# Kernel tuning notes

Measured on AMD Instinct MI355X. Metric: run time of the kernel, lower is better.

The kernel has to match this reference:

```python
import jax, jax.numpy as jnp
import numpy as np

N_MAP, N_ACT, B, E_PER, D = 131072, 1024, 16, 16384, 128
MAP_PER, ACT_PER = N_MAP // B, N_ACT // B
E = B * E_PER
EPS = 1e-5  # torch GroupNorm default eps


def _gn(x, g, b):
    # GroupNorm(1, C) on [N, C]: per-row normalization over channels
    m = jnp.mean(x, -1, keepdims=True)
    v = jnp.mean((x - m) ** 2, -1, keepdims=True)
    return (x - m) * jax.lax.rsqrt(v + EPS) * g + b


def _lin_gn(x, W, g, b, act=True):
    # LaneGCN Linear: nn.Linear(bias=False) -> GroupNorm(1, n_out) -> optional ReLU
    y = _gn(x @ W.T, g, b)
    return jax.nn.relu(y) if act else y


def setup_inputs() -> dict:
    key = jax.random.key(0)
    keys = iter(jax.random.split(key, 64))
    nrm = lambda shape, s=1.0: jax.random.normal(next(keys), shape, jnp.float32) * s
    uni = lambda shape, s=1.0: jax.random.uniform(next(keys), shape, jnp.float32) * s
    inp = {}
    inp['feat'] = nrm((N_MAP, D))
    inp['turn'] = nrm((N_MAP, 2))
    inp['control'] = uni((N_MAP,))
    inp['intersect'] = uni((N_MAP,))
    inp['map_ctrs'] = uni((N_MAP, 2), 100.0)
    inp['actors'] = nrm((N_ACT, D))
    inp['actor_ctrs'] = uni((N_ACT, 2), 100.0)
    # fixed within-scene edge list (stands in for the distance-threshold nonzero)
    rng = np.random.default_rng(0)
    hi = np.concatenate([rng.integers(b * MAP_PER, (b + 1) * MAP_PER, E_PER) for b in range(B)])
    wi = np.concatenate([rng.integers(b * ACT_PER, (b + 1) * ACT_PER, E_PER) for b in range(B)])
    inp['hi'] = jnp.asarray(hi, jnp.int32)
    inp['wi'] = jnp.asarray(wi, jnp.int32)
    # parameters
    W = lambda *s: nrm(s, 0.02)
    g_ = lambda *s: 1.0 + nrm(s, 0.05)
    b_ = lambda *s: nrm(s, 0.05)
    inp['meta_W'], inp['meta_g'], inp['meta_b'] = W(D, D + 4), g_(D), b_(D)
    inp['dW1'], inp['db1'] = W(2, D, 2), b_(2, D)
    inp['dW2'], inp['dg2'], inp['dbt2'] = W(2, D, D), g_(2, D), b_(2, D)
    inp['qW'], inp['qg'], inp['qb'] = W(2, D, D), g_(2, D), b_(2, D)
    inp['cW1'], inp['cg1'], inp['cb1'] = W(2, D, 3 * D), g_(2, D), b_(2, D)
    inp['cW2'] = W(2, D, D)
    inp['aW'] = W(2, D, D)
    inp['ng_g'], inp['ng_b'] = g_(2, D), b_(2, D)
    inp['lW'], inp['lg'], inp['lb'] = W(2, D, D), g_(2, D), b_(2, D)
    return inp


def reference(feat, turn, control, intersect, map_ctrs, actors, actor_ctrs, hi, wi,
              meta_W, meta_g, meta_b, dW1, db1, dW2, dg2, dbt2, qW, qg, qb,
              cW1, cg1, cb1, cW2, aW, ng_g, ng_b, lW, lg, lb):
    # meta fuse: concat(feat, turn, control, intersect) -> Linear+GN+ReLU
    meta = jnp.concatenate([feat, turn, control[:, None], intersect[:, None]], axis=1)
    feat = _lin_gn(meta, meta_W, meta_g, meta_b)
    for i in range(2):  # two Att blocks
        res = feat
        # dist branch: raw ctr offsets -> Linear(2,n_ctx)+ReLU -> Linear+GN+ReLU
        d = map_ctrs[hi] - actor_ctrs[wi]                       # [E, 2]
        d = jax.nn.relu(d @ dW1[i].T + db1[i])                  # [E, D]
        d = _lin_gn(d, dW2[i], dg2[i], dbt2[i])
        q = _lin_gn(feat[hi], qW[i], qg[i], qb[i])              # query on gathered agts
        c = jnp.concatenate([d, q, actors[wi]], axis=1)         # [E, 3D]
        c = _lin_gn(c, cW1[i], cg1[i], cb1[i])
        c = c @ cW2[i].T                                        # bias-free Linear
        a = feat @ aW[i].T                                      # self path, bias-free
        a = a.at[hi].add(c)                                     # scatter-add messages
        a = jax.nn.relu(_gn(a, ng_g[i], ng_b[i]))
        a = _lin_gn(a, lW[i], lg[i], lb[i], act=False)
        feat = jax.nn.relu(a + res)                             # use_relu=True
    return feat
```

## Files before the change

kernel.cpp:

```cpp
#include <hip/hip_runtime.h>
#include <stdint.h>

typedef unsigned short u16;
typedef __bf16 bf16x8 __attribute__((ext_vector_type(8)));
typedef float f32x4 __attribute__((ext_vector_type(4)));

#define MFMA(a, b, c) __builtin_amdgcn_mfma_f32_16x16x32_bf16(a, b, c, 0, 0, 0)

__device__ __forceinline__ u16 f2bf(float f) {
    union { float f; unsigned u; } v; v.f = f;
    unsigned r = v.u + 0x7fffu + ((v.u >> 16) & 1u);
    return (u16)(r >> 16);
}
__device__ __forceinline__ float bf2f(u16 h) {
    union { unsigned u; float f; } v; v.u = ((unsigned)h) << 16; return v.f;
}
__device__ __forceinline__ bf16x8 as_frag(uint4 u) {
    union { uint4 u; bf16x8 b; } v; v.u = u; return v.b;
}
__device__ __forceinline__ bf16x8 ldg_frag(const u16* p) {
    return as_frag(*reinterpret_cast<const uint4*>(p));
}
__device__ __forceinline__ int rowmap(int t, int i) {
    return 32 * (t >> 1) + 8 * (i >> 2) + 4 * (t & 1) + (i & 3);
}

template <int SRC_LDU>
__device__ __forceinline__ void stage128(const u16* __restrict__ src, u16* dst, int tid, int nt) {
    for (int c = tid; c < 2048; c += nt) {
        int row = c >> 4, j = c & 15;
        int js = (j & 8) | ((j ^ row) & 7);
        *reinterpret_cast<uint4*>(dst + row * 128 + js * 8) =
            *reinterpret_cast<const uint4*>(src + row * SRC_LDU + j * 8);
    }
}
__device__ __forceinline__ bf16x8 lds_w(const u16* base, int row, int byteoff) {
    int off = row * 256 + (byteoff ^ ((row & 7) << 4));
    return as_frag(*reinterpret_cast<const uint4*>(reinterpret_cast<const char*>(base) + off));
}

template <int KT>
__device__ __forceinline__ void gemm_acc(const bf16x8* a, const u16* __restrict__ W, int ldw,
                                         f32x4* acc, int c16, int q4) {
#pragma unroll
    for (int n = 0; n < 8; n++) {
        const u16* wp = W + (size_t)(n * 16 + c16) * ldw + q4 * 8;
#pragma unroll
        for (int k = 0; k < KT; k++) {
            bf16x8 b = ldg_frag(wp + k * 32);
            acc[n] = MFMA(a[k], b, acc[n]);
        }
    }
}

__device__ __forceinline__ void gn_t(f32x4* acc, const float* __restrict__ gb, bool relu, int q4) {
    float s = 0.f, s2 = 0.f;
#pragma unroll
    for (int t = 0; t < 8; t++)
#pragma unroll
        for (int r = 0; r < 4; r++) { float x = acc[t][r]; s += x; s2 = fmaf(x, x, s2); }
    s += __shfl_xor(s, 16, 64); s += __shfl_xor(s, 32, 64);
    s2 += __shfl_xor(s2, 16, 64); s2 += __shfl_xor(s2, 32, 64);
    float mean = s * (1.f / 128.f);
    float var = fmaf(s2, 1.f / 128.f, -mean * mean);
    float rstd = rsqrtf(var + 1e-5f);
#pragma unroll
    for (int t = 0; t < 8; t++) {
        const float4* g4 = reinterpret_cast<const float4*>(gb + (t * 16 + q4 * 4) * 2);
        float4 p01 = g4[0], p23 = g4[1];
        float gv[4] = {p01.x, p01.z, p23.x, p23.z};
        float bv[4] = {p01.y, p01.w, p23.y, p23.w};
#pragma unroll
        for (int r = 0; r < 4; r++) {
            float y = fmaf((acc[t][r] - mean) * rstd, gv[r], bv[r]);
            acc[t][r] = relu ? fmaxf(y, 0.f) : y;
        }
    }
}

__device__ __forceinline__ bf16x8 pack_frag(f32x4 lo, f32x4 hi) {
    union { u16 s[8]; bf16x8 b; } t;
#pragma unroll
    for (int j = 0; j < 4; j++) { t.s[j] = f2bf(lo[j]); t.s[4 + j] = f2bf(hi[j]); }
    return t.b;
}

__device__ __forceinline__ void gn_c(f32x4* acc, const float* __restrict__ g,
                                     const float* __restrict__ b, bool relu, int c16) {
    float gs[8], bs[8];
#pragma unroll
    for (int n = 0; n < 8; n++) { gs[n] = g[n * 16 + c16]; bs[n] = b[n * 16 + c16]; }
#pragma unroll
    for (int r = 0; r < 4; r++) {
        float s = 0.f, s2 = 0.f;
#pragma unroll
        for (int n = 0; n < 8; n++) { float x = acc[n][r]; s += x; s2 = fmaf(x, x, s2); }
#pragma unroll
        for (int m = 1; m < 16; m <<= 1) { s += __shfl_xor(s, m, 64); s2 += __shfl_xor(s2, m, 64); }
        float mean = s * (1.f / 128.f);
        float var = fmaf(s2, 1.f / 128.f, -mean * mean);
        float rstd = rsqrtf(var + 1e-5f);
#pragma unroll
        for (int n = 0; n < 8; n++) {
            float y = fmaf((acc[n][r] - mean) * rstd, gs[n], bs[n]);
            acc[n][r] = relu ? fmaxf(y, 0.f) : y;
        }
    }
}

__global__ __launch_bounds__(256) void k_prep(
    const float* __restrict__ dW2s, const float* __restrict__ qWs, const float* __restrict__ cW1s,
    const float* __restrict__ cW2s, const float* __restrict__ aWs, const float* __restrict__ lWs,
    const float* __restrict__ metaW,
    const float* __restrict__ dW1s, const float* __restrict__ db1s,
    const float* __restrict__ dg2s, const float* __restrict__ dbt2s,
    const float* __restrict__ qgs, const float* __restrict__ qbs,
    const float* __restrict__ cg1s, const float* __restrict__ cb1s,
    u16* __restrict__ o_dW2p, u16* __restrict__ o_qWp, u16* __restrict__ o_cW10,
    u16* __restrict__ o_cW1q, u16* __restrict__ o_cW1a,
    u16* __restrict__ o_cW2, u16* __restrict__ o_aW, u16* __restrict__ o_lW,
    u16* __restrict__ o_mWf, float* __restrict__ o_mWe,
    float* __restrict__ o_dw1p, float* __restrict__ o_gb) {
    int idx = blockIdx.x * 256 + threadIdx.x;
    if (idx >= 281600) return;
    if (idx < 32768) {
        int i = idx >> 14, rem = idx & 16383, ro = rem >> 7, col = rem & 127;
        o_dW2p[idx] = f2bf(dW2s[i * 16384 + rowmap(ro >> 4, ro & 15) * 128 + col]);
    } else if (idx < 65536) {
        int j = idx - 32768, i = j >> 14, rem = j & 16383, ro = rem >> 7, col = rem & 127;
        o_qWp[j] = f2bf(qWs[i * 16384 + rowmap(ro >> 4, ro & 15) * 128 + col]);
    } else if (idx < 98304) {
        int j = idx - 65536, i = j >> 14, rem = j & 16383, ro = rem >> 7, col = rem & 127;
        o_cW10[j] = f2bf(cW1s[i * 49152 + rowmap(ro >> 4, ro & 15) * 384 + col]);
    } else if (idx < 131072) {
        int j = idx - 98304, i = j >> 14, rem = j & 16383, ro = rem >> 7, col = rem & 127;
        o_cW1q[j] = f2bf(cW1s[i * 49152 + rowmap(ro >> 4, ro & 15) * 384 + 128 + col]);
    } else if (idx < 163840) {
        int j = idx - 131072, i = j >> 14, rem = j & 16383, ro = rem >> 7, col = rem & 127;
        o_cW1a[j] = f2bf(cW1s[i * 49152 + rowmap(ro >> 4, ro & 15) * 384 + 256 + col]);
    } else if (idx < 196608) { int j = idx - 163840; o_cW2[j] = f2bf(cW2s[j]); }
    else if (idx < 229376) { int j = idx - 196608; o_aW[j] = f2bf(aWs[j]); }
    else if (idx < 262144) { int j = idx - 229376; o_lW[j] = f2bf(lWs[j]); }
    else if (idx < 278528) { int j = idx - 262144; o_mWf[j] = f2bf(metaW[(j >> 7) * 132 + (j & 127)]); }
    else if (idx < 279040) { int j = idx - 278528; o_mWe[j] = metaW[(j >> 2) * 132 + 128 + (j & 3)]; }
    else if (idx < 280064) {
        int j = idx - 279040, i = j >> 9, col = (j >> 2) & 127, t = j & 3;
        float v = (t == 0) ? dW1s[i * 256 + col * 2]
                : (t == 1) ? dW1s[i * 256 + col * 2 + 1]
                : (t == 2) ? db1s[i * 128 + col] : 0.f;
        o_dw1p[j] = v;
    } else {
        int j = idx - 280064;
        int tb = j >> 9, rem = j & 511, i = rem >> 8, q = rem & 255, o = q >> 1, f = q & 1;
        const float* gsrc = (tb == 0) ? dg2s : (tb == 1) ? qgs : cg1s;
        const float* bsrc = (tb == 0) ? dbt2s : (tb == 1) ? qbs : cb1s;
        int src = i * 128 + rowmap(o >> 4, o & 15);
        o_gb[j] = f ? bsrc[src] : gsrc[src];
    }
}

__global__ __launch_bounds__(256) void k_meta(
    const float* __restrict__ feat, const float* __restrict__ turn,
    const float* __restrict__ ctrl, const float* __restrict__ inter,
    const u16* __restrict__ mWf, const float* __restrict__ mWe,
    const float* __restrict__ g, const float* __restrict__ b, u16* __restrict__ out) {
    int lane = threadIdx.x & 63, wv = threadIdx.x >> 6;
    int c16 = lane & 15, q4 = lane >> 4;
    int m0 = (blockIdx.x * 4 + wv) * 16;
    bf16x8 a[4];
    const float* xr = feat + (size_t)(m0 + c16) * 128 + q4 * 8;
#pragma unroll
    for (int k = 0; k < 4; k++) {
        float4 u0 = *reinterpret_cast<const float4*>(xr + k * 32);
        float4 u1 = *reinterpret_cast<const float4*>(xr + k * 32 + 4);
        union { u16 s[8]; bf16x8 b; } t;
        t.s[0] = f2bf(u0.x); t.s[1] = f2bf(u0.y); t.s[2] = f2bf(u0.z); t.s[3] = f2bf(u0.w);
        t.s[4] = f2bf(u1.x); t.s[5] = f2bf(u1.y); t.s[6] = f2bf(u1.z); t.s[7] = f2bf(u1.w);
        a[k] = t.b;
    }
    f32x4 acc[8] = {};
    gemm_acc<4>(a, mWf, 128, acc, c16, q4);
#pragma unroll
    for (int r = 0; r < 4; r++) {
        int row = m0 + q4 * 4 + r;
        float t0 = turn[2 * row], t1 = turn[2 * row + 1];
        float cv = ctrl[row], iv = inter[row];
#pragma unroll
        for (int n = 0; n < 8; n++) {
            int col = n * 16 + c16;
            float4 we = reinterpret_cast<const float4*>(mWe)[col];
            acc[n][r] += t0 * we.x + t1 * we.y + cv * we.z + iv * we.w;
        }
    }
    gn_c(acc, g, b, true, c16);
#pragma unroll
    for (int r = 0; r < 4; r++) {
        size_t row = m0 + q4 * 4 + r;
#pragma unroll
        for (int n = 0; n < 8; n++) out[row * 128 + n * 16 + c16] = f2bf(acc[n][r]);
    }
}

__global__ __launch_bounds__(256) void k_act(
    const float* __restrict__ actors, const u16* __restrict__ cW1ap, u16* __restrict__ ac_out) {
    int lane = threadIdx.x & 63, wv = threadIdx.x >> 6;
    int c16 = lane & 15, q4 = lane >> 4;
    int b = (int)blockIdx.x;
    int i = b >> 4;
    int row = ((b & 15) * 4 + wv) * 16 + c16;
    const float* xr = actors + (size_t)row * 128 + q4 * 8;
    bf16x8 f[4];
#pragma unroll
    for (int k = 0; k < 4; k++) {
        union { u16 s[8]; uint4 u; } t;
#pragma unroll
        for (int j = 0; j < 8; j++) t.s[j] = f2bf(xr[k * 32 + j]);
        f[k] = as_frag(t.u);
    }
    const u16* Wp = cW1ap + i * 16384;
    f32x4 acc[8] = {};
#pragma unroll
    for (int k = 0; k < 4; k++)
#pragma unroll
        for (int t = 0; t < 8; t++) {
            bf16x8 a = ldg_frag(Wp + (size_t)(t * 16 + c16) * 128 + k * 32 + q4 * 8);
            acc[t] = MFMA(a, f[k], acc[t]);
        }
    u16* dst = ac_out + (size_t)i * 131072 + (size_t)row * 128 + q4 * 8;
#pragma unroll
    for (int T = 0; T < 4; T++) {
        bf16x8 p = pack_frag(acc[2 * T], acc[2 * T + 1]);
        union { bf16x8 b; uint4 u; } v; v.b = p;
        *reinterpret_cast<uint4*>(dst + T * 32) = v.u;
    }
}

__global__ __launch_bounds__(256) void k_nodeA(
    const u16* __restrict__ featb, const u16* __restrict__ qWp, const u16* __restrict__ aW,
    const float* __restrict__ gb_q, const u16* __restrict__ cW1qp,
    u16* __restrict__ qc_out, float* __restrict__ a_out) {
    int lane = threadIdx.x & 63, wv = threadIdx.x >> 6;
    int c16 = lane & 15, q4 = lane >> 4;
    int m0 = (blockIdx.x * 4 + wv) * 16;
    bf16x8 f[4];
    const u16* xr = featb + (size_t)(m0 + c16) * 128 + q4 * 8;
#pragma unroll
    for (int k = 0; k < 4; k++) f[k] = ldg_frag(xr + k * 32);
    f32x4 acca[8] = {};
    gemm_acc<4>(f, aW, 128, acca, c16, q4);
#pragma unroll
    for (int r = 0; r < 4; r++) {
        size_t row = m0 + q4 * 4 + r;
#pragma unroll
        for (int n = 0; n < 8; n++) a_out[row * 128 + n * 16 + c16] = acca[n][r];
    }
    f32x4 accq[8] = {};
#pragma unroll
    for (int k = 0; k < 4; k++)
#pragma unroll
        for (int t = 0; t < 8; t++) {
            bf16x8 a = ldg_frag(qWp + (size_t)(t * 16 + c16) * 128 + k * 32 + q4 * 8);
            accq[t] = MFMA(a, f[k], accq[t]);
        }
    gn_t(accq, gb_q, true, q4);
    bf16x8 qf[4];
#pragma unroll
    for (int k = 0; k < 4; k++) qf[k] = pack_frag(accq[2 * k], accq[2 * k + 1]);
    f32x4 acc2[8] = {};
#pragma unroll
    for (int k = 0; k < 4; k++)
#pragma unroll
        for (int t = 0; t < 8; t++) {
            bf16x8 a = ldg_frag(cW1qp + (size_t)(t * 16 + c16) * 128 + k * 32 + q4 * 8);
            acc2[t] = MFMA(a, qf[k], acc2[t]);
        }
    u16* dst = qc_out + (size_t)(m0 + c16) * 128 + q4 * 8;
#pragma unroll
    for (int T = 0; T < 4; T++) {
        bf16x8 p = pack_frag(acc2[2 * T], acc2[2 * T + 1]);
        union { bf16x8 b; uint4 u; } v; v.b = p;
        *reinterpret_cast<uint4*>(dst + T * 32) = v.u;
    }
}

__global__ __launch_bounds__(256) void k_edge(
    const int* __restrict__ hi, const int* __restrict__ wi,
    const float* __restrict__ mctr, const float* __restrict__ actr,
    const float* __restrict__ dw1p, const u16* __restrict__ dW2p,
    const float* __restrict__ gb_d2,
    const u16* __restrict__ qc, const u16* __restrict__ ac,
    const u16* __restrict__ cW10p, const float* __restrict__ gb_c1,
    const u16* __restrict__ cW2, float* __restrict__ a_out) {
    __shared__ u16 s0[16384];
    int tid = threadIdx.x;
    int lane = tid & 63, wv = tid >> 6;
    int c16 = lane & 15, q4 = lane >> 4;
    int bid = (int)blockIdx.x;
    bid = (bid & 7) * 256 + (bid >> 3);
    int ebase = bid * 128 + wv * 32;
    int h0 = hi[ebase + c16], w0 = wi[ebase + c16];
    int h1 = hi[ebase + 16 + c16], w1 = wi[ebase + 16 + c16];
    stage128<128>(dW2p, s0, tid, 256);
    union F8 { bf16x8 b; uint4 u; u16 s[8]; };
    F8 qg0[4], qg1[4], ag0[4], ag1[4];
#pragma unroll
    for (int T = 0; T < 4; T++) {
        qg0[T].b = ldg_frag(qc + (size_t)h0 * 128 + T * 32 + q4 * 8);
        qg1[T].b = ldg_frag(qc + (size_t)h1 * 128 + T * 32 + q4 * 8);
        ag0[T].b = ldg_frag(ac + (size_t)w0 * 128 + T * 32 + q4 * 8);
        ag1[T].b = ldg_frag(ac + (size_t)w1 * 128 + T * 32 + q4 * 8);
    }
    float dx0 = mctr[2 * h0] - actr[2 * w0], dy0 = mctr[2 * h0 + 1] - actr[2 * w0 + 1];
    float dx1 = mctr[2 * h1] - actr[2 * w1], dy1 = mctr[2 * h1 + 1] - actr[2 * w1 + 1];
    bf16x8 bd0[4], bd1[4];
    const float4* w4p = reinterpret_cast<const float4*>(dw1p);
#pragma unroll
    for (int k = 0; k < 4; k++) {
        union { u16 s[8]; uint4 u; } t0, t1;
#pragma unroll
        for (int j = 0; j < 8; j++) {
            float4 w4 = w4p[k * 32 + q4 * 8 + j];
            t0.s[j] = f2bf(fmaxf(fmaf(dx0, w4.x, fmaf(dy0, w4.y, w4.z)), 0.f));
            t1.s[j] = f2bf(fmaxf(fmaf(dx1, w4.x, fmaf(dy1, w4.y, w4.z)), 0.f));
        }
        bd0[k] = as_frag(t0.u); bd1[k] = as_frag(t1.u);
    }
    __syncthreads();
    f32x4 accA[8] = {}, accB[8] = {};
#pragma unroll
    for (int k = 0; k < 4; k++)
#pragma unroll
        for (int t = 0; t < 8; t++) {
            bf16x8 a = lds_w(s0, t * 16 + c16, k * 64 + q4 * 16);
            accA[t] = MFMA(a, bd0[k], accA[t]);
            accB[t] = MFMA(a, bd1[k], accB[t]);
        }
    gn_t(accA, gb_d2, true, q4);
    gn_t(accB, gb_d2, true, q4);
    bf16x8 d2f0[4], d2f1[4];
#pragma unroll
    for (int k = 0; k < 4; k++) {
        d2f0[k] = pack_frag(accA[2 * k], accA[2 * k + 1]);
        d2f1[k] = pack_frag(accB[2 * k], accB[2 * k + 1]);
    }
    __syncthreads();
    stage128<128>(cW10p, s0, tid, 256);
    __syncthreads();
    f32x4 cA[8] = {}, cB[8] = {};
#pragma unroll
    for (int k = 0; k < 4; k++)
#pragma unroll
        for (int t = 0; t < 8; t++) {
            bf16x8 a = lds_w(s0, t * 16 + c16, k * 64 + q4 * 16);
            cA[t] = MFMA(a, d2f0[k], cA[t]);
            cB[t] = MFMA(a, d2f1[k], cB[t]);
        }
#pragma unroll
    for (int t = 0; t < 8; t++) {
        int T = t >> 1, base = 4 * (t & 1);
#pragma unroll
        for (int r = 0; r < 4; r++) {
            cA[t][r] += bf2f(qg0[T].s[base + r]) + bf2f(ag0[T].s[base + r]);
            cB[t][r] += bf2f(qg1[T].s[base + r]) + bf2f(ag1[T].s[base + r]);
        }
    }
    gn_t(cA, gb_c1, true, q4);
    gn_t(cB, gb_c1, true, q4);
    bf16x8 ba0[4], ba1[4];
#pragma unroll
    for (int k = 0; k < 4; k++) {
        ba0[k] = pack_frag(cA[2 * k], cA[2 * k + 1]);
        ba1[k] = pack_frag(cB[2 * k], cB[2 * k + 1]);
    }
    __syncthreads();
    stage128<128>(cW2, s0, tid, 256);
    __syncthreads();
    f32x4 oA[8] = {}, oB[8] = {};
#pragma unroll
    for (int k = 0; k < 4; k++)
#pragma unroll
        for (int n = 0; n < 8; n++) {
            bf16x8 b = lds_w(s0, n * 16 + c16, k * 64 + q4 * 16);
            oA[n] = MFMA(ba0[k], b, oA[n]);
            oB[n] = MFMA(ba1[k], b, oB[n]);
        }
#pragma unroll
    for (int r = 0; r < 4; r++) {
        int hr0 = hi[ebase + q4 * 4 + r];
        int hr1 = hi[ebase + 16 + q4 * 4 + r];
        float* dst0 = a_out + (size_t)hr0 * 128 + c16;
        float* dst1 = a_out + (size_t)hr1 * 128 + c16;
#pragma unroll
        for (int n = 0; n < 8; n++) {
            unsafeAtomicAdd(dst0 + n * 16, oA[n][r]);
            unsafeAtomicAdd(dst1 + n * 16, oB[n][r]);
        }
    }
}

__global__ __launch_bounds__(256) void k_nodeB(
    const float* __restrict__ a_in, const float* __restrict__ gg, const float* __restrict__ gb,
    const u16* __restrict__ lW, const float* __restrict__ lg, const float* __restrict__ lb,
    const u16* __restrict__ res, u16* __restrict__ out_bf, float* __restrict__ out_f32) {
    int lane = threadIdx.x & 63, wv = threadIdx.x >> 6;
    int c16 = lane & 15, q4 = lane >> 4;
    int m0 = (blockIdx.x * 4 + wv) * 16;
    const float* xr = a_in + (size_t)(m0 + c16) * 128 + q4 * 8;
    float x[32];
#pragma unroll
    for (int k = 0; k < 4; k++) {
        float4 u0 = *reinterpret_cast<const float4*>(xr + k * 32);
        float4 u1 = *reinterpret_cast<const float4*>(xr + k * 32 + 4);
        x[k * 8 + 0] = u0.x; x[k * 8 + 1] = u0.y; x[k * 8 + 2] = u0.z; x[k * 8 + 3] = u0.w;
        x[k * 8 + 4] = u1.x; x[k * 8 + 5] = u1.y; x[k * 8 + 6] = u1.z; x[k * 8 + 7] = u1.w;
    }
    float s = 0.f, s2 = 0.f;
#pragma unroll
    for (int t = 0; t < 32; t++) { s += x[t]; s2 = fmaf(x[t], x[t], s2); }
    s += __shfl_xor(s, 16, 64); s += __shfl_xor(s, 32, 64);
    s2 += __shfl_xor(s2, 16, 64); s2 += __shfl_xor(s2, 32, 64);
    float mean = s * (1.f / 128.f);
    float var = fmaf(s2, 1.f / 128.f, -mean * mean);
    float rstd = rsqrtf(var + 1e-5f);
    bf16x8 a[4];
#pragma unroll
    for (int k = 0; k < 4; k++) {
        float4 g0 = *reinterpret_cast<const float4*>(gg + k * 32 + q4 * 8);
        float4 g1 = *reinterpret_cast<const float4*>(gg + k * 32 + q4 * 8 + 4);
        float4 b0 = *reinterpret_cast<const float4*>(gb + k * 32 + q4 * 8);
        float4 b1 = *reinterpret_cast<const float4*>(gb + k * 32 + q4 * 8 + 4);
        float gv[8] = {g0.x, g0.y, g0.z, g0.w, g1.x, g1.y, g1.z, g1.w};
        float bv[8] = {b0.x, b0.y, b0.z, b0.w, b1.x, b1.y, b1.z, b1.w};
        union { u16 s[8]; bf16x8 b; } t;
#pragma unroll
        for (int j = 0; j < 8; j++) {
            float y = fmaf((x[k * 8 + j] - mean) * rstd, gv[j], bv[j]);
            t.s[j] = f2bf(fmaxf(y, 0.f));
        }
        a[k] = t.b;
    }
    f32x4 acc[8] = {};
    gemm_acc<4>(a, lW, 128, acc, c16, q4);
    gn_c(acc, lg, lb, false, c16);
#pragma unroll
    for (int r = 0; r < 4; r++) {
        size_t row = m0 + q4 * 4 + r;
#pragma unroll
        for (int n = 0; n < 8; n++) {
            int col = n * 16 + c16;
            float y = acc[n][r] + bf2f(res[row * 128 + col]);
            y = fmaxf(y, 0.f);
            if (out_bf) out_bf[row * 128 + col] = f2bf(y);
            else out_f32[row * 128 + col] = y;
        }
    }
}

extern "C" void kernel_launch(void* const* d_in, const int* in_sizes, int n_in,
                              void* d_out, int out_size, void* d_ws, size_t ws_size,
                              hipStream_t stream) {
    const float* feat = (const float*)d_in[0];
    const float* turn = (const float*)d_in[1];
    const float* ctrl = (const float*)d_in[2];
    const float* inter = (const float*)d_in[3];
    const float* mctr = (const float*)d_in[4];
    const float* actors = (const float*)d_in[5];
    const float* actr = (const float*)d_in[6];
    const int* hi = (const int*)d_in[7];
    const int* wi = (const int*)d_in[8];
    const float* metaW = (const float*)d_in[9];
    const float* metag = (const float*)d_in[10];
    const float* metab = (const float*)d_in[11];
    const float* dW1 = (const float*)d_in[12];
    const float* db1 = (const float*)d_in[13];
    const float* dW2 = (const float*)d_in[14];
    const float* dg2 = (const float*)d_in[15];
    const float* dbt2 = (const float*)d_in[16];
    const float* qW = (const float*)d_in[17];
    const float* qg = (const float*)d_in[18];
    const float* qb = (const float*)d_in[19];
    const float* cW1 = (const float*)d_in[20];
    const float* cg1 = (const float*)d_in[21];
    const float* cb1 = (const float*)d_in[22];
    const float* cW2 = (const float*)d_in[23];
    const float* aW = (const float*)d_in[24];
    const float* ngg = (const float*)d_in[25];
    const float* ngb = (const float*)d_in[26];
    const float* lW = (const float*)d_in[27];
    const float* lg = (const float*)d_in[28];
    const float* lb = (const float*)d_in[29];

    char* ws = (char*)d_ws;
    u16* feat0 = (u16*)(ws);
    u16* feat1 = (u16*)(ws + 33554432);
    u16* qcbuf = (u16*)(ws + 67108864);
    u16* acbuf = (u16*)(ws + 100663296);
    u16* wdW2p = (u16*)(ws + 101187584);
    u16* wqWp = (u16*)(ws + 101253120);
    u16* wcW10 = (u16*)(ws + 101318656);
    u16* wcW1q = (u16*)(ws + 101384192);
    u16* wcW1a = (u16*)(ws + 101449728);
    u16* wcW2 = (u16*)(ws + 101515264);
    u16* waW = (u16*)(ws + 101580800);
    u16* wlW = (u16*)(ws + 101646336);
    u16* wmWf = (u16*)(ws + 101711872);
    float* wmWe = (float*)(ws + 101744640);
    float* wdw1p = (float*)(ws + 101746688);
    float* gball = (float*)(ws + 101750784);
    float* abuf = (float*)d_out;

    k_prep<<<1100, 256, 0, stream>>>(dW2, qW, cW1, cW2, aW, lW, metaW, dW1, db1,
                                     dg2, dbt2, qg, qb, cg1, cb1,
                                     wdW2p, wqWp, wcW10, wcW1q, wcW1a, wcW2, waW, wlW,
                                     wmWf, wmWe, wdw1p, gball);
    k_meta<<<2048, 256, 0, stream>>>(feat, turn, ctrl, inter, wmWf, wmWe, metag, metab, feat0);
    k_act<<<32, 256, 0, stream>>>(actors, wcW1a, acbuf);
    for (int i = 0; i < 2; i++) {
        const u16* fcur = i ? feat1 : feat0;
        k_nodeA<<<2048, 256, 0, stream>>>(fcur, wqWp + i * 16384, waW + i * 16384,
                                          gball + 512 + i * 256, wcW1q + i * 16384,
                                          qcbuf, abuf);
        k_edge<<<2048, 256, 0, stream>>>(hi, wi, mctr, actr, wdw1p + i * 512, wdW2p + i * 16384,
                                         gball + i * 256, qcbuf, acbuf + i * 131072,
                                         wcW10 + i * 16384, gball + 1024 + i * 256,
                                         wcW2 + i * 16384, abuf);
        k_nodeB<<<2048, 256, 0, stream>>>(abuf, ngg + i * 128, ngb + i * 128, wlW + i * 16384,
                                          lg + i * 128, lb + i * 128, fcur,
                                          i ? nullptr : feat1, i ? (float*)d_out : nullptr);
    }
}
```

Baseline: 704.1 us.

## Accumulate scatter buffer in bf16 with packed bf16 atomics, reuse feat buffers

The node accumulator `a` changes from fp32 to bf16. The self-path kernel writes bf16, and the edge kernel scatters messages with global_atomic_pk_add_bf16. Lane pairs exchange values by shuffle so each atomic carries two adjacent channels. This halves the number of atomic operations and the bytes moved through the scatter buffer and the following GroupNorm read. The buffer is aliased onto the idle feature ping-pong buffer, so the normalization kernel now updates it in place. The cost is accuracy: repeated bf16 rounding during accumulation can drift from the fp32 reference.

```diff
diff --git a/kernel.cpp b/kernel.cpp
--- a/kernel.cpp
+++ b/kernel.cpp
@@ -238,7 +238,7 @@
 __global__ __launch_bounds__(256) void k_nodeA(
     const u16* __restrict__ featb, const u16* __restrict__ qWp, const u16* __restrict__ aW,
     const float* __restrict__ gb_q, const u16* __restrict__ cW1qp,
-    u16* __restrict__ qc_out, float* __restrict__ a_out) {
+    u16* __restrict__ qc_out, u16* __restrict__ a_out) {
     int lane = threadIdx.x & 63, wv = threadIdx.x >> 6;
     int c16 = lane & 15, q4 = lane >> 4;
     int m0 = (blockIdx.x * 4 + wv) * 16;
@@ -252,7 +252,7 @@
     for (int r = 0; r < 4; r++) {
         size_t row = m0 + q4 * 4 + r;
 #pragma unroll
-        for (int n = 0; n < 8; n++) a_out[row * 128 + n * 16 + c16] = acca[n][r];
+        for (int n = 0; n < 8; n++) a_out[row * 128 + n * 16 + c16] = f2bf(acca[n][r]);
     }
     f32x4 accq[8] = {};
 #pragma unroll
@@ -290,7 +290,7 @@
     const float* __restrict__ gb_d2,
     const u16* __restrict__ qc, const u16* __restrict__ ac,
     const u16* __restrict__ cW10p, const float* __restrict__ gb_c1,
-    const u16* __restrict__ cW2, float* __restrict__ a_out) {
+    const u16* __restrict__ cW2, u16* __restrict__ a_out) {
     __shared__ u16 s0[16384];
     int tid = threadIdx.x;
     int lane = tid & 63, wv = tid >> 6;
@@ -388,31 +388,42 @@
     for (int r = 0; r < 4; r++) {
         int hr0 = hi[ebase + q4 * 4 + r];
         int hr1 = hi[ebase + 16 + q4 * 4 + r];
-        float* dst0 = a_out + (size_t)hr0 * 128 + c16;
-        float* dst1 = a_out + (size_t)hr1 * 128 + c16;
+        u16* d0 = a_out + (size_t)hr0 * 128 + (c16 & ~1);
+        u16* d1 = a_out + (size_t)hr1 * 128 + (c16 & ~1);
 #pragma unroll
         for (int n = 0; n < 8; n++) {
-            unsafeAtomicAdd(dst0 + n * 16, oA[n][r]);
-            unsafeAtomicAdd(dst1 + n * 16, oB[n][r]);
+            float pA = __shfl_xor(oA[n][r], 1, 64);
+            float pB = __shfl_xor(oB[n][r], 1, 64);
+            bool even = !(c16 & 1);
+            float loA = even ? oA[n][r] : pA, hiA = even ? pA : oA[n][r];
+            float loB = even ? oB[n][r] : pB, hiB = even ? pB : oB[n][r];
+            unsigned pkA = (unsigned)f2bf(loA) | ((unsigned)f2bf(hiA) << 16);
+            unsigned pkB = (unsigned)f2bf(loB) | ((unsigned)f2bf(hiB) << 16);
+            if ((n & 1) == (c16 & 1)) {
+                asm volatile("global_atomic_pk_add_bf16 %0, %1, off"
+                             :: "v"(d0 + n * 16), "v"(pkA) : "memory");
+                asm volatile("global_atomic_pk_add_bf16 %0, %1, off"
+                             :: "v"(d1 + n * 16), "v"(pkB) : "memory");
+            }
         }
     }
 }
 
 __global__ __launch_bounds__(256) void k_nodeB(
-    const float* __restrict__ a_in, const float* __restrict__ gg, const float* __restrict__ gb,
+    const u16* a_in, const float* __restrict__ gg, const float* __restrict__ gb,
     const u16* __restrict__ lW, const float* __restrict__ lg, const float* __restrict__ lb,
-    const u16* __restrict__ res, u16* __restrict__ out_bf, float* __restrict__ out_f32) {
+    const u16* __restrict__ res, u16* out_bf, float* __restrict__ out_f32) {
     int lane = threadIdx.x & 63, wv = threadIdx.x >> 6;
     int c16 = lane & 15, q4 = lane >> 4;
     int m0 = (blockIdx.x * 4 + wv) * 16;
-    const float* xr = a_in + (size_t)(m0 + c16) * 128 + q4 * 8;
+    const u16* xr = a_in + (size_t)(m0 + c16) * 128 + q4 * 8;
     float x[32];
 #pragma unroll
     for (int k = 0; k < 4; k++) {
-        float4 u0 = *reinterpret_cast<const float4*>(xr + k * 32);
-        float4 u1 = *reinterpret_cast<const float4*>(xr + k * 32 + 4);
-        x[k * 8 + 0] = u0.x; x[k * 8 + 1] = u0.y; x[k * 8 + 2] = u0.z; x[k * 8 + 3] = u0.w;
-        x[k * 8 + 4] = u1.x; x[k * 8 + 5] = u1.y; x[k * 8 + 6] = u1.z; x[k * 8 + 7] = u1.w;
+        union { uint4 u; u16 s[8]; } v;
+        v.u = *reinterpret_cast<const uint4*>(xr + k * 32);
+#pragma unroll
+        for (int j = 0; j < 8; j++) x[k * 8 + j] = bf2f(v.s[j]);
     }
     float s = 0.f, s2 = 0.f;
 #pragma unroll
@@ -507,7 +518,6 @@
     float* wmWe = (float*)(ws + 101744640);
     float* wdw1p = (float*)(ws + 101746688);
     float* gball = (float*)(ws + 101750784);
-    float* abuf = (float*)d_out;
 
     k_prep<<<1100, 256, 0, stream>>>(dW2, qW, cW1, cW2, aW, lW, metaW, dW1, db1,
                                      dg2, dbt2, qg, qb, cg1, cb1,
@@ -517,6 +527,7 @@
     k_act<<<32, 256, 0, stream>>>(actors, wcW1a, acbuf);
     for (int i = 0; i < 2; i++) {
         const u16* fcur = i ? feat1 : feat0;
+        u16* abuf = i ? feat0 : feat1;
         k_nodeA<<<2048, 256, 0, stream>>>(fcur, wqWp + i * 16384, waW + i * 16384,
                                           gball + 512 + i * 256, wcW1q + i * 16384,
                                           qcbuf, abuf);
```

Measured after the change: 704.7 us, median of 2. Within noise of the previous version (+0.1%).
